# Performance work log

Hardware: AMD Instinct MI355X
Metric: run time of the kernel (lower is better)

## Reference

```python
import jax, jax.numpy as jnp
import numpy as np

N = 8192        # args.network_verNum (nodes)
T = 6           # args.pick_T_num (snapshots)
STEP = 3        # timesteps between consecutive picks


def setup_inputs() -> dict:
    key = jax.random.key(0)
    k1, k2, k3 = jax.random.split(key, 3)
    # adjacency mask (~avg degree 16) and IC-style edge probabilities, as in reset_parameters
    adj = jax.random.uniform(k1, (N, N)) < 0.002
    vals = jnp.array([0.03, 0.05, 0.07, 0.1, 0.12], dtype=jnp.float32)
    idx = jax.random.randint(k2, (N, N), 0, 5)
    weight = jnp.where(adj, vals[idx], 0.0).astype(jnp.float32)
    # monotone 0/1 activation snapshots [T, N]
    snaps = (jax.random.uniform(k3, (T, N)) < 0.05).astype(jnp.float32)
    snaps = jnp.clip(jnp.cumsum(snaps, axis=0), 0.0, 1.0)
    time_pick = np.arange(T, dtype=np.int64) * STEP
    return {"snapshot_vec_series": snaps, "weight": weight, "time_pick": time_pick}


def reference(snapshot_vec_series, weight, time_pick):
    # snapshot_vec_series: [T, N] float; weight: [N, N] float; time_pick: [T] static ints
    tp = np.asarray(time_pick)
    Tn = snapshot_vec_series.shape[0]

    def step(rv, _):
        # P2[i, j] = weight[j, i] * rv[j]; neg_mul[i] = prod_j (1 - P2[i, j])
        neg_mul = jnp.prod(1.0 - weight * rv[:, None], axis=0)  # [N]
        return 1.0 - neg_mul, None

    outs = []
    for T_index in range(1, Tn - 1):
        rv = snapshot_vec_series[T_index] - snapshot_vec_series[T_index - 1]  # newly activated
        n_steps = int(tp[T_index + 1] - tp[T_index])
        rv, _ = jax.lax.scan(step, rv, None, length=n_steps)
        outs.append(rv)
    return jnp.stack(outs)  # [T-2, N]
```

## Files before the change

### kernel.cpp

```cpp
#include <hip/hip_runtime.h>
#include <hip/hip_bf16.h>


#define CAP 64

typedef float floatx4 __attribute__((ext_vector_type(4)));

template <bool POW2>
__global__ __launch_bounds__(256) void build_edges_kernel(
    const floatx4* __restrict__ W4, unsigned total4, unsigned log2N, unsigned maskN,
    int* __restrict__ cnt, uint2* __restrict__ epk, unsigned N) {
    const unsigned gsize = gridDim.x * blockDim.x;
    unsigned e4 = blockIdx.x * blockDim.x + threadIdx.x;

    unsigned s0w = 0, s0j = 0, s0i = 0;
    unsigned s1w = 0, s1j = 0, s1i = 0;
    int scnt = 0;

    auto collect = [&](float w, unsigned j, unsigned i) {
        if (scnt == 0)      { s0w = __float_as_uint(w); s0j = j; s0i = i; scnt = 1; }
        else if (scnt == 1) { s1w = __float_as_uint(w); s1j = j; s1i = i; scnt = 2; }
        else {
            int k = atomicAdd(&cnt[i], 1);
            if (k < CAP) {
                uint2 p; p.x = __float_as_uint(w); p.y = j;
                epk[(unsigned)k * N + i] = p;
            }
        }
    };

    auto process = [&](floatx4 v, unsigned e) {
        unsigned ored = __float_as_uint(v.x) | __float_as_uint(v.y) |
                        __float_as_uint(v.z) | __float_as_uint(v.w);
        if (ored == 0u) return;
        unsigned j, i0;
        if (POW2) { j = e >> log2N; i0 = e & maskN; }
        else      { j = e / N;      i0 = e - j * N; }
#pragma unroll
        for (int t = 0; t < 4; ++t) {
            float w = v[t];
            if (w != 0.0f) collect(w, j, i0 + t);
        }
    };

    for (; e4 + 7u * gsize < total4; e4 += 8u * gsize) {
        floatx4 v0 = W4[e4];
        floatx4 v1 = W4[e4 + gsize];
        floatx4 v2 = W4[e4 + 2u * gsize];
        floatx4 v3 = W4[e4 + 3u * gsize];
        floatx4 v4 = W4[e4 + 4u * gsize];
        floatx4 v5 = W4[e4 + 5u * gsize];
        floatx4 v6 = W4[e4 + 6u * gsize];
        floatx4 v7 = W4[e4 + 7u * gsize];
        process(v0, (e4) << 2);
        process(v1, (e4 + gsize) << 2);
        process(v2, (e4 + 2u * gsize) << 2);
        process(v3, (e4 + 3u * gsize) << 2);
        process(v4, (e4 + 4u * gsize) << 2);
        process(v5, (e4 + 5u * gsize) << 2);
        process(v6, (e4 + 6u * gsize) << 2);
        process(v7, (e4 + 7u * gsize) << 2);
    }
    for (; e4 < total4; e4 += gsize) process(W4[e4], e4 << 2);

    if (scnt >= 1) {
        int k = atomicAdd(&cnt[s0i], 1);
        if (k < CAP) { uint2 p; p.x = s0w; p.y = s0j; epk[(unsigned)k * N + s0i] = p; }
    }
    if (scnt >= 2) {
        int k = atomicAdd(&cnt[s1i], 1);
        if (k < CAP) { uint2 p; p.x = s1w; p.y = s1j; epk[(unsigned)k * N + s1i] = p; }
    }
}

template <bool FIRST>
__global__ __launch_bounds__(128) void step_kernel(
    const float* __restrict__ rv_in,
    const float* __restrict__ snaps,
    float* __restrict__ rv_out,
    const int* __restrict__ cnt,
    const uint2* __restrict__ epk,
    int N) {
    const int c = blockIdx.y;
    const int i = blockIdx.x * blockDim.x + threadIdx.x;
    if (i >= N) return;
    const float* rv = rv_in + (size_t)c * N;
    const float* sa = snaps + (size_t)(c + 1) * N;
    const float* sb = snaps + (size_t)c * N;
    int n = cnt[i];
    if (n > CAP) n = CAP;
    float prod = 1.0f;
#pragma unroll 4
    for (int k = 0; k < n; ++k) {
        uint2 p = epk[(size_t)k * N + i];
        float w = __uint_as_float(p.x);
        int j = (int)p.y;
        float r = FIRST ? (sa[j] - sb[j]) : rv[j];
        prod *= 1.0f - w * r;
    }
    rv_out[(size_t)c * N + i] = 1.0f - prod;
}

extern "C" void kernel_launch(void* const* d_in, const int* in_sizes, int n_in,
                              void* d_out, int out_size, void* d_ws, size_t ws_size,
                              hipStream_t stream) {
    const float* snaps = (const float*)d_in[0];
    const float* W     = (const float*)d_in[1];

    const int T = in_sizes[2];
    const int N = in_sizes[0] / T;
    const int chains = T - 2;
    const int NSTEPS = 3;

    char* ws = (char*)d_ws;
    int*   cnt = (int*)ws;
    size_t off = ((size_t)N * 4 + 255) & ~(size_t)255;
    float* rvA = (float*)(ws + off);
    off += ((size_t)chains * N * 4 + 255) & ~(size_t)255;
    float* rvB = (float*)(ws + off);
    off += ((size_t)chains * N * 4 + 255) & ~(size_t)255;
    uint2* epk = (uint2*)(ws + off);

    hipMemsetAsync(cnt, 0, (size_t)N * sizeof(int), stream);

    const unsigned total4 = (unsigned)((size_t)N * N / 4);
    const bool pow2 = (N & (N - 1)) == 0;
    unsigned log2N = 0;
    while ((1u << log2N) < (unsigned)N) ++log2N;
    const int bblk = 256;
    int bgrd = (int)((total4 + (unsigned)bblk * 32 - 1) / ((unsigned)bblk * 32));
    if (bgrd < 1) bgrd = 1;
    if (pow2)
        build_edges_kernel<true><<<bgrd, bblk, 0, stream>>>(
            (const floatx4*)W, total4, log2N, (unsigned)N - 1, cnt, epk, (unsigned)N);
    else
        build_edges_kernel<false><<<bgrd, bblk, 0, stream>>>(
            (const floatx4*)W, total4, log2N, (unsigned)N - 1, cnt, epk, (unsigned)N);

    const int sblk = 128;
    dim3 sgrd((N + sblk - 1) / sblk, chains);
    float* outp = (float*)d_out;

    float* out0 = (NSTEPS == 1) ? outp : rvA;
    step_kernel<true><<<sgrd, sblk, 0, stream>>>(nullptr, snaps, out0, cnt, epk, N);
    float* bufs[2] = {rvA, rvB};
    for (int s = 1; s < NSTEPS; ++s) {
        const float* in = bufs[(s - 1) & 1];
        float* out = (s == NSTEPS - 1) ? outp : bufs[s & 1];
        step_kernel<false><<<sgrd, sblk, 0, stream>>>(in, nullptr, out, cnt, epk, N);
    }
}
```

Measured before the change: 78.75 us.

## Buffer edges in shared memory per block and use 32-lane groups per node

The edge-building kernel now queues nonzero edges in a per-block shared-memory buffer and flushes them to the global CSR-like lists after the scan, instead of holding two edges per thread in registers. The block grid doubles while each thread's unroll drops from 8 to 4 loads. The step kernel assigns a 32-lane group per node, strides over its edges and reduces the product with xor shuffles. The intent is more memory parallelism in the dense weight scan and lower latency per node in the sparse step. It also packs j and i into 16 bits each, which assumes N <= 65536, and on a 64-wide wavefront most lanes sit idle for degree ~16.

New measurement: 70.83 us. -10.1%, faster.

```diff
diff --git a/kernel.cpp b/kernel.cpp
--- a/kernel.cpp
+++ b/kernel.cpp
@@ -2,7 +2,8 @@
 #include <hip/hip_bf16.h>
 
 
-#define CAP 64
+#define CAP  64
+#define QMAX 128
 
 typedef float floatx4 __attribute__((ext_vector_type(4)));
 
@@ -10,25 +11,26 @@
 __global__ __launch_bounds__(256) void build_edges_kernel(
     const floatx4* __restrict__ W4, unsigned total4, unsigned log2N, unsigned maskN,
     int* __restrict__ cnt, uint2* __restrict__ epk, unsigned N) {
+    __shared__ unsigned qcount;
+    __shared__ unsigned qw[QMAX];
+    __shared__ unsigned qji[QMAX];
+    if (threadIdx.x == 0) qcount = 0u;
+    __syncthreads();
+
     const unsigned gsize = gridDim.x * blockDim.x;
     unsigned e4 = blockIdx.x * blockDim.x + threadIdx.x;
 
-    unsigned s0w = 0, s0j = 0, s0i = 0;
-    unsigned s1w = 0, s1j = 0, s1i = 0;
-    int scnt = 0;
-
-    auto collect = [&](float w, unsigned j, unsigned i) {
-        if (scnt == 0)      { s0w = __float_as_uint(w); s0j = j; s0i = i; scnt = 1; }
-        else if (scnt == 1) { s1w = __float_as_uint(w); s1j = j; s1i = i; scnt = 2; }
-        else {
-            int k = atomicAdd(&cnt[i], 1);
-            if (k < CAP) {
-                uint2 p; p.x = __float_as_uint(w); p.y = j;
-                epk[(unsigned)k * N + i] = p;
-            }
+    auto emit = [&](float w, unsigned j, unsigned i) {
+        unsigned k = atomicAdd(&qcount, 1u);
+        if (k < QMAX) {
+            qw[k]  = __float_as_uint(w);
+            qji[k] = (j << 16) | i;
+        } else {
+            int s = atomicAdd(&cnt[i], 1);
+            if (s < CAP) { uint2 p; p.x = __float_as_uint(w); p.y = j;
+                           epk[(unsigned)s * N + i] = p; }
         }
     };
-
     auto process = [&](floatx4 v, unsigned e) {
         unsigned ored = __float_as_uint(v.x) | __float_as_uint(v.y) |
                         __float_as_uint(v.z) | __float_as_uint(v.w);
@@ -37,52 +39,45 @@
         if (POW2) { j = e >> log2N; i0 = e & maskN; }
         else      { j = e / N;      i0 = e - j * N; }
 #pragma unroll
-        for (int t = 0; t < 4; ++t) {
-            float w = v[t];
-            if (w != 0.0f) collect(w, j, i0 + t);
-        }
+        for (int t = 0; t < 4; ++t)
+            if (v[t] != 0.0f) emit(v[t], j, i0 + t);
     };
 
-    for (; e4 + 7u * gsize < total4; e4 += 8u * gsize) {
+    for (; e4 + 3u * gsize < total4; e4 += 4u * gsize) {
         floatx4 v0 = W4[e4];
         floatx4 v1 = W4[e4 + gsize];
         floatx4 v2 = W4[e4 + 2u * gsize];
         floatx4 v3 = W4[e4 + 3u * gsize];
-        floatx4 v4 = W4[e4 + 4u * gsize];
-        floatx4 v5 = W4[e4 + 5u * gsize];
-        floatx4 v6 = W4[e4 + 6u * gsize];
-        floatx4 v7 = W4[e4 + 7u * gsize];
         process(v0, (e4) << 2);
         process(v1, (e4 + gsize) << 2);
         process(v2, (e4 + 2u * gsize) << 2);
         process(v3, (e4 + 3u * gsize) << 2);
-        process(v4, (e4 + 4u * gsize) << 2);
-        process(v5, (e4 + 5u * gsize) << 2);
-        process(v6, (e4 + 6u * gsize) << 2);
-        process(v7, (e4 + 7u * gsize) << 2);
     }
     for (; e4 < total4; e4 += gsize) process(W4[e4], e4 << 2);
 
-    if (scnt >= 1) {
-        int k = atomicAdd(&cnt[s0i], 1);
-        if (k < CAP) { uint2 p; p.x = s0w; p.y = s0j; epk[(unsigned)k * N + s0i] = p; }
-    }
-    if (scnt >= 2) {
-        int k = atomicAdd(&cnt[s1i], 1);
-        if (k < CAP) { uint2 p; p.x = s1w; p.y = s1j; epk[(unsigned)k * N + s1i] = p; }
+    __syncthreads();
+    unsigned qn = qcount < (unsigned)QMAX ? qcount : (unsigned)QMAX;
+    for (unsigned t = threadIdx.x; t < qn; t += blockDim.x) {
+        unsigned wbits = qw[t], ji = qji[t];
+        unsigned i = ji & 0xffffu, j = ji >> 16;
+        int s = atomicAdd(&cnt[i], 1);
+        if (s < CAP) { uint2 p; p.x = wbits; p.y = j;
+                       epk[(unsigned)s * N + i] = p; }
     }
 }
 
 template <bool FIRST>
-__global__ __launch_bounds__(128) void step_kernel(
+__global__ __launch_bounds__(256) void step_lp_kernel(
     const float* __restrict__ rv_in,
     const float* __restrict__ snaps,
     float* __restrict__ rv_out,
     const int* __restrict__ cnt,
     const uint2* __restrict__ epk,
     int N) {
-    const int c = blockIdx.y;
-    const int i = blockIdx.x * blockDim.x + threadIdx.x;
+    const int c    = blockIdx.y;
+    const int lane = threadIdx.x & 31;
+    const int grp  = threadIdx.x >> 5;
+    const int i    = blockIdx.x * 8 + grp;
     if (i >= N) return;
     const float* rv = rv_in + (size_t)c * N;
     const float* sa = snaps + (size_t)(c + 1) * N;
@@ -90,15 +85,15 @@
     int n = cnt[i];
     if (n > CAP) n = CAP;
     float prod = 1.0f;
-#pragma unroll 4
-    for (int k = 0; k < n; ++k) {
+    for (int k = lane; k < n; k += 32) {
         uint2 p = epk[(size_t)k * N + i];
         float w = __uint_as_float(p.x);
         int j = (int)p.y;
         float r = FIRST ? (sa[j] - sb[j]) : rv[j];
         prod *= 1.0f - w * r;
     }
-    rv_out[(size_t)c * N + i] = 1.0f - prod;
+    for (int off = 16; off; off >>= 1) prod *= __shfl_xor(prod, off, 32);
+    if (lane == 0) rv_out[(size_t)c * N + i] = 1.0f - prod;
 }
 
 extern "C" void kernel_launch(void* const* d_in, const int* in_sizes, int n_in,
@@ -128,7 +123,7 @@
     unsigned log2N = 0;
     while ((1u << log2N) < (unsigned)N) ++log2N;
     const int bblk = 256;
-    int bgrd = (int)((total4 + (unsigned)bblk * 32 - 1) / ((unsigned)bblk * 32));
+    int bgrd = (int)((total4 + (unsigned)bblk * 16 - 1) / ((unsigned)bblk * 16));
     if (bgrd < 1) bgrd = 1;
     if (pow2)
         build_edges_kernel<true><<<bgrd, bblk, 0, stream>>>(
@@ -137,16 +132,15 @@
         build_edges_kernel<false><<<bgrd, bblk, 0, stream>>>(
             (const floatx4*)W, total4, log2N, (unsigned)N - 1, cnt, epk, (unsigned)N);
 
-    const int sblk = 128;
-    dim3 sgrd((N + sblk - 1) / sblk, chains);
+    dim3 sgrd((N + 7) / 8, chains);
     float* outp = (float*)d_out;
 
     float* out0 = (NSTEPS == 1) ? outp : rvA;
-    step_kernel<true><<<sgrd, sblk, 0, stream>>>(nullptr, snaps, out0, cnt, epk, N);
+    step_lp_kernel<true><<<sgrd, 256, 0, stream>>>(nullptr, snaps, out0, cnt, epk, N);
     float* bufs[2] = {rvA, rvB};
     for (int s = 1; s < NSTEPS; ++s) {
         const float* in = bufs[(s - 1) & 1];
         float* out = (s == NSTEPS - 1) ? outp : bufs[s & 1];
-        step_kernel<false><<<sgrd, sblk, 0, stream>>>(in, nullptr, out, cnt, epk, N);
+        step_lp_kernel<false><<<sgrd, 256, 0, stream>>>(in, nullptr, out, cnt, epk, N);
     }
 }
```
